# Kernel tuning notes

Hardware: AMD Instinct MI355X
Metric: run time of the kernel (lower is better)

## Reference

```python
import jax, jax.numpy as jnp
import numpy as np

N = 16777216  # length of the returns series


def setup_inputs() -> dict:
    key = jax.random.key(0)
    returns = 0.01 * jax.random.normal(key, (N,), dtype=jnp.float32)
    return {
        "returns": returns,
        "omega": jnp.float32(0.01),
        "alpha": jnp.float32(0.1),
        "beta": jnp.float32(0.85),
    }


def reference(returns, omega, alpha, beta):
    # GARCH(1,1): h[0] = var(returns) (unbiased, matching torch.var default);
    # h[t] = omega + alpha * r[t-1]^2 + beta * h[t-1]
    h0 = jnp.var(returns, ddof=1)
    # drivers b_t = omega + alpha * r_{t-1}^2 for t = 1..n-1
    b = omega + alpha * jnp.square(returns[:-1])

    def step(h_prev, b_t):
        h_t = b_t + beta * h_prev
        return h_t, h_t

    _, h_rest = jax.lax.scan(step, h0, b)
    h = jnp.concatenate([h0[None], h_rest])  # [n]
    return jnp.sqrt(h), h
```

## Files before the change

kernel.cpp:

```cpp
#include <hip/hip_runtime.h>
#include <math.h>


#define VAR_BLOCKS 1024
#define KPW 4096
#define MAIN_BLOCK 256

__global__ void var_partial(const float* __restrict__ r, int n,
                            double* __restrict__ partial) {
    int tid = blockIdx.x * blockDim.x + threadIdx.x;
    int stride = gridDim.x * blockDim.x;
    double s = 0.0, q = 0.0;
    int n4 = n >> 2;
    const float4* r4 = (const float4*)r;
    for (int i = tid; i < n4; i += stride) {
        float4 v = r4[i];
        s += (double)v.x + (double)v.y + (double)v.z + (double)v.w;
        q += (double)v.x * v.x + (double)v.y * v.y
           + (double)v.z * v.z + (double)v.w * v.w;
    }
    for (int i = (n4 << 2) + tid; i < n; i += stride) {
        double v = r[i];
        s += v; q += v * v;
    }
    for (int d = 1; d < 64; d <<= 1) {
        s += __shfl_xor(s, d, 64);
        q += __shfl_xor(q, d, 64);
    }
    __shared__ double ls[4], lq[4];
    int wid = threadIdx.x >> 6, lane = threadIdx.x & 63;
    if (lane == 0) { ls[wid] = s; lq[wid] = q; }
    __syncthreads();
    if (threadIdx.x == 0) {
        double S = 0.0, Q = 0.0;
        for (int w = 0; w < (int)(blockDim.x >> 6); ++w) { S += ls[w]; Q += lq[w]; }
        partial[2 * blockIdx.x]     = S;
        partial[2 * blockIdx.x + 1] = Q;
    }
}

__global__ void var_final(const double* __restrict__ partial, int nblocks, int n,
                          float* __restrict__ h0_out) {
    double s = 0.0, q = 0.0;
    for (int i = threadIdx.x; i < nblocks; i += blockDim.x) {
        s += partial[2 * i];
        q += partial[2 * i + 1];
    }
    for (int d = 1; d < 64; d <<= 1) {
        s += __shfl_xor(s, d, 64);
        q += __shfl_xor(q, d, 64);
    }
    __shared__ double ls[4], lq[4];
    int wid = threadIdx.x >> 6, lane = threadIdx.x & 63;
    if (lane == 0) { ls[wid] = s; lq[wid] = q; }
    __syncthreads();
    if (threadIdx.x == 0) {
        double S = 0.0, Q = 0.0;
        for (int w = 0; w < (int)(blockDim.x >> 6); ++w) { S += ls[w]; Q += lq[w]; }
        double mean = S / (double)n;
        double var = (Q - (double)n * mean * mean) / (double)(n - 1);
        *h0_out = (float)var;
    }
}

__global__ __launch_bounds__(MAIN_BLOCK)
void garch_main(const float* __restrict__ r, int n,
                const float* __restrict__ pOmega, const float* __restrict__ pAlpha,
                const float* __restrict__ pBeta, const float* __restrict__ pH0,
                float* __restrict__ out_sqrt, float* __restrict__ out_h) {
    const int lane = threadIdx.x & 63;
    const int gwave = (blockIdx.x * blockDim.x + threadIdx.x) >> 6;
    const int start = gwave * KPW;
    if (start >= n) return;

    const float omega = *pOmega;
    const float alpha = *pAlpha;
    const float beta  = *pBeta;
    const float h0    = *pH0;

    const float c1 = beta;
    const float c2 = c1 * c1;
    const float c3 = c2 * c1;
    const float c4 = c2 * c2;
    const float c8 = c4 * c4;
    const float c16 = c8 * c8;
    const float c32 = c16 * c16;
    const float c64 = c32 * c32;
    const float c128 = c64 * c64;

    float pw1 = 1.0f;
    {
        float p = beta; int e = lane;
        if (e & 1)  pw1 *= p; p *= p;
        if (e & 2)  pw1 *= p; p *= p;
        if (e & 4)  pw1 *= p; p *= p;
        if (e & 8)  pw1 *= p; p *= p;
        if (e & 16) pw1 *= p; p *= p;
        if (e & 32) pw1 *= p;
    }
    float pw4 = 1.0f;
    {
        float p = c4; int e = lane;
        if (e & 1)  pw4 *= p; p *= p;
        if (e & 2)  pw4 *= p; p *= p;
        if (e & 4)  pw4 *= p; p *= p;
        if (e & 8)  pw4 *= p; p *= p;
        if (e & 16) pw4 *= p; p *= p;
        if (e & 32) pw4 *= p;
    }

    float h_prev, r_carry;
    if (start == 0) {
        h_prev = 0.0f;
        r_carry = 0.0f;
    } else {
        float ra = r[start - 2 - lane];
        float rb = r[start - 66 - lane];
        float ba = fmaf(alpha * ra, ra, omega);
        float bb = fmaf(alpha * rb, rb, omega);
        float part = pw1 * fmaf(c64, bb, ba);
        for (int d = 1; d < 64; d <<= 1) part += __shfl_xor(part, d, 64);
        h_prev = part;
        r_carry = r[start - 1];
    }

    int end = start + KPW; if (end > n) end = n;
    const float4* r4p = (const float4*)r;

    int s = start;
    for (; s + 256 <= end; s += 256) {
        float4 rv = r4p[(s >> 2) + lane];
        float prev = __shfl_up(rv.w, 1, 64);
        if (lane == 0) prev = r_carry;

        float b0 = fmaf(alpha * prev, prev, omega);
        float b1 = fmaf(alpha * rv.x, rv.x, omega);
        float b2 = fmaf(alpha * rv.y, rv.y, omega);
        float b3 = fmaf(alpha * rv.z, rv.z, omega);
        if (s == 0 && lane == 0) b0 = h0;

        float B = fmaf(c1, b2, b3);
        B = fmaf(c2, b1, B);
        B = fmaf(c3, b0, B);

        float t;
        t = __shfl_up(B, 1, 64);  if (lane >= 1)  B = fmaf(c4,  t, B);
        t = __shfl_up(B, 2, 64);  if (lane >= 2)  B = fmaf(c8,  t, B);
        t = __shfl_up(B, 4, 64);  if (lane >= 4)  B = fmaf(c16, t, B);
        t = __shfl_up(B, 8, 64);  if (lane >= 8)  B = fmaf(c32, t, B);
        t = __shfl_up(B, 16, 64); if (lane >= 16) B = fmaf(c64, t, B);
        t = __shfl_up(B, 32, 64); if (lane >= 32) B = fmaf(c128, t, B);

        float Bex = __shfl_up(B, 1, 64);
        if (lane == 0) Bex = 0.0f;
        float h_base = fmaf(pw4, h_prev, Bex);

        float h0v = fmaf(c1, h_base, b0);
        float h1v = fmaf(c1, h0v, b1);
        float h2v = fmaf(c1, h1v, b2);
        float h3v = fmaf(c1, h2v, b3);

        int idx4 = (s >> 2) + lane;
        float4 hs = make_float4(h0v, h1v, h2v, h3v);
        float4 sq = make_float4(sqrtf(h0v), sqrtf(h1v), sqrtf(h2v), sqrtf(h3v));
        reinterpret_cast<float4*>(out_sqrt)[idx4] = sq;
        reinterpret_cast<float4*>(out_h)[idx4]    = hs;

        h_prev  = __shfl(h3v, 63, 64);
        r_carry = __shfl(rv.w, 63, 64);
    }

    if (s < end && lane == 0) {
        float h = h_prev;
        for (int tt = s; tt < end; ++tt) {
            float rr = (tt > 0) ? r[tt - 1] : 0.0f;
            float b = fmaf(alpha * rr, rr, omega);
            float hv = (tt == 0) ? h0 : fmaf(beta, h, b);
            out_sqrt[tt] = sqrtf(hv);
            out_h[tt] = hv;
            h = hv;
        }
    }
}

extern "C" void kernel_launch(void* const* d_in, const int* in_sizes, int n_in,
                              void* d_out, int out_size, void* d_ws, size_t ws_size,
                              hipStream_t stream) {
    const float* r      = (const float*)d_in[0];
    const float* pOmega = (const float*)d_in[1];
    const float* pAlpha = (const float*)d_in[2];
    const float* pBeta  = (const float*)d_in[3];
    int n = in_sizes[0];

    float* out_sqrt = (float*)d_out;
    float* out_h    = out_sqrt + n;

    double* partial = (double*)d_ws;
    float* h0p = (float*)((char*)d_ws + 2 * VAR_BLOCKS * sizeof(double));

    var_partial<<<VAR_BLOCKS, 256, 0, stream>>>(r, n, partial);
    var_final<<<1, 256, 0, stream>>>(partial, VAR_BLOCKS, n, h0p);

    int elems_per_block = KPW * (MAIN_BLOCK / 64);
    int nblocks = (n + elems_per_block - 1) / elems_per_block;
    garch_main<<<nblocks, MAIN_BLOCK, 0, stream>>>(
        r, n, pOmega, pAlpha, pBeta, h0p, out_sqrt, out_h);
}
```

Baseline: 196.9 us.

## Fuse variance reduction into scan pass and patch the h0-dependent prefix afterward

Drops the separate variance pre-pass so the input is read once. The scan kernel now also accumulates the sum and sum of squares. It runs with h0 treated as zero, and a single-block finalize kernel computes the variance and serially recomputes the first 256 outputs, where beta^t*h0 still matters in float. Each wave now handles 8 elements per lane with nontemporal stores. The risk is that truncating the h0 correction at 256 steps relies on beta^256 being negligible, which holds for typical beta but is not exact in general.

```diff
diff --git a/kernel.cpp b/kernel.cpp
--- a/kernel.cpp
+++ b/kernel.cpp
@@ -2,34 +2,161 @@
 #include <math.h>
 
 
-#define VAR_BLOCKS 1024
-#define KPW 4096
+#define KPW 2048
 #define MAIN_BLOCK 256
-
-__global__ void var_partial(const float* __restrict__ r, int n,
-                            double* __restrict__ partial) {
-    int tid = blockIdx.x * blockDim.x + threadIdx.x;
-    int stride = gridDim.x * blockDim.x;
-    double s = 0.0, q = 0.0;
-    int n4 = n >> 2;
-    const float4* r4 = (const float4*)r;
-    for (int i = tid; i < n4; i += stride) {
-        float4 v = r4[i];
-        s += (double)v.x + (double)v.y + (double)v.z + (double)v.w;
-        q += (double)v.x * v.x + (double)v.y * v.y
-           + (double)v.z * v.z + (double)v.w * v.w;
-    }
-    for (int i = (n4 << 2) + tid; i < n; i += stride) {
-        double v = r[i];
-        s += v; q += v * v;
-    }
+#define FIX 256
+
+typedef float v4f __attribute__((ext_vector_type(4)));
+
+__global__ __launch_bounds__(MAIN_BLOCK, 6)
+void garch_fused(const float* __restrict__ r, int n,
+                 const float* __restrict__ pOmega, const float* __restrict__ pAlpha,
+                 const float* __restrict__ pBeta,
+                 float* __restrict__ out_sqrt, float* __restrict__ out_h,
+                 double* __restrict__ partial) {
+    const int lane = threadIdx.x & 63;
+    const int wid  = threadIdx.x >> 6;
+    const int gwave = (blockIdx.x * blockDim.x + threadIdx.x) >> 6;
+    const int start = gwave * KPW;
+
+    const float omega = *pOmega;
+    const float alpha = *pAlpha;
+    const float beta  = *pBeta;
+
+    const float c1 = beta;
+    const float c2 = c1 * c1;
+    const float c3 = c2 * c1;
+    const float c4 = c2 * c2;
+    const float c8 = c4 * c4;
+    const float c16 = c8 * c8;
+    const float c32 = c16 * c16;
+    const float c64 = c32 * c32;
+    const float c128 = c64 * c64;
+    const float c256 = c128 * c128;
+
+    double acc_s = 0.0, acc_q = 0.0;
+
+    if (start < n) {
+        float pw1 = 1.0f;
+        { float p = c1; int e = lane;
+          if (e & 1)  pw1 *= p; p *= p;
+          if (e & 2)  pw1 *= p; p *= p;
+          if (e & 4)  pw1 *= p; p *= p;
+          if (e & 8)  pw1 *= p; p *= p;
+          if (e & 16) pw1 *= p; p *= p;
+          if (e & 32) pw1 *= p; }
+        float pw8 = 1.0f;
+        { float p = c8; int e = lane;
+          if (e & 1)  pw8 *= p; p *= p;
+          if (e & 2)  pw8 *= p; p *= p;
+          if (e & 4)  pw8 *= p; p *= p;
+          if (e & 8)  pw8 *= p; p *= p;
+          if (e & 16) pw8 *= p; p *= p;
+          if (e & 32) pw8 *= p; }
+
+        float h_prev, r_carry;
+        if (start == 0) {
+            h_prev = 0.0f;
+            r_carry = 0.0f;
+        } else {
+            float ra = r[start - 2 - lane];
+            float rb = r[start - 66 - lane];
+            float ba = fmaf(alpha * ra, ra, omega);
+            float bb = fmaf(alpha * rb, rb, omega);
+            float part = pw1 * fmaf(c64, bb, ba);
+            for (int d = 1; d < 64; d <<= 1) part += __shfl_xor(part, d, 64);
+            h_prev = part;
+            r_carry = r[start - 1];
+        }
+
+        int end = start + KPW; if (end > n) end = n;
+        const float4* r4p = (const float4*)r;
+
+        int s = start;
+        for (; s + 512 <= end; s += 512) {
+            int idx4 = (s >> 2) + 2 * lane;
+            float4 ra = r4p[idx4];
+            float4 rb = r4p[idx4 + 1];
+
+            float sf = ((ra.x + ra.y) + (ra.z + ra.w)) + ((rb.x + rb.y) + (rb.z + rb.w));
+            float qf = fmaf(ra.x, ra.x, fmaf(ra.y, ra.y, fmaf(ra.z, ra.z, ra.w * ra.w)));
+            qf = fmaf(rb.x, rb.x, fmaf(rb.y, rb.y, fmaf(rb.z, rb.z, fmaf(rb.w, rb.w, qf))));
+            acc_s += (double)sf;
+            acc_q += (double)qf;
+
+            float prev = __shfl_up(rb.w, 1, 64);
+            if (lane == 0) prev = r_carry;
+
+            float b0 = fmaf(alpha * prev, prev, omega);
+            float b1 = fmaf(alpha * ra.x, ra.x, omega);
+            float b2 = fmaf(alpha * ra.y, ra.y, omega);
+            float b3 = fmaf(alpha * ra.z, ra.z, omega);
+            float b4 = fmaf(alpha * ra.w, ra.w, omega);
+            float b5 = fmaf(alpha * rb.x, rb.x, omega);
+            float b6 = fmaf(alpha * rb.y, rb.y, omega);
+            float b7 = fmaf(alpha * rb.z, rb.z, omega);
+            if (s == 0 && lane == 0) b0 = 0.0f;
+
+            float lo = fmaf(c1, b2, b3); lo = fmaf(c2, b1, lo); lo = fmaf(c3, b0, lo);
+            float B  = fmaf(c1, b6, b7); B  = fmaf(c2, b5, B);  B  = fmaf(c3, b4, B);
+            B = fmaf(c4, lo, B);
+
+            float t;
+            t = __shfl_up(B, 1, 64);  if (lane >= 1)  B = fmaf(c8,   t, B);
+            t = __shfl_up(B, 2, 64);  if (lane >= 2)  B = fmaf(c16,  t, B);
+            t = __shfl_up(B, 4, 64);  if (lane >= 4)  B = fmaf(c32,  t, B);
+            t = __shfl_up(B, 8, 64);  if (lane >= 8)  B = fmaf(c64,  t, B);
+            t = __shfl_up(B, 16, 64); if (lane >= 16) B = fmaf(c128, t, B);
+            t = __shfl_up(B, 32, 64); if (lane >= 32) B = fmaf(c256, t, B);
+
+            float Bex = __shfl_up(B, 1, 64);
+            if (lane == 0) Bex = 0.0f;
+            float h_base = fmaf(pw8, h_prev, Bex);
+
+            float h0v = fmaf(c1, h_base, b0);
+            float h1v = fmaf(c1, h0v, b1);
+            float h2v = fmaf(c1, h1v, b2);
+            float h3v = fmaf(c1, h2v, b3);
+            float h4v = fmaf(c1, h3v, b4);
+            float h5v = fmaf(c1, h4v, b5);
+            float h6v = fmaf(c1, h5v, b6);
+            float h7v = fmaf(c1, h6v, b7);
+
+            v4f hA = {h0v, h1v, h2v, h3v};
+            v4f hB = {h4v, h5v, h6v, h7v};
+            v4f sA = {sqrtf(h0v), sqrtf(h1v), sqrtf(h2v), sqrtf(h3v)};
+            v4f sB = {sqrtf(h4v), sqrtf(h5v), sqrtf(h6v), sqrtf(h7v)};
+            __builtin_nontemporal_store(hA, (v4f*)out_h + idx4);
+            __builtin_nontemporal_store(hB, (v4f*)out_h + idx4 + 1);
+            __builtin_nontemporal_store(sA, (v4f*)out_sqrt + idx4);
+            __builtin_nontemporal_store(sB, (v4f*)out_sqrt + idx4 + 1);
+
+            h_prev  = __shfl(h7v, 63, 64);
+            r_carry = __shfl(rb.w, 63, 64);
+        }
+
+        if (s < end && lane == 0) {
+            float h = h_prev;
+            for (int tt = s; tt < end; ++tt) {
+                float rr = (tt > 0) ? r[tt - 1] : 0.0f;
+                float b = fmaf(alpha * rr, rr, omega);
+                float hv = (tt == 0) ? 0.0f : fmaf(beta, h, b);
+                out_sqrt[tt] = sqrtf(hv);
+                out_h[tt] = hv;
+                h = hv;
+                float rv = r[tt];
+                acc_s += (double)rv;
+                acc_q += (double)rv * rv;
+            }
+        }
+    }
+
     for (int d = 1; d < 64; d <<= 1) {
-        s += __shfl_xor(s, d, 64);
-        q += __shfl_xor(q, d, 64);
-    }
-    __shared__ double ls[4], lq[4];
-    int wid = threadIdx.x >> 6, lane = threadIdx.x & 63;
-    if (lane == 0) { ls[wid] = s; lq[wid] = q; }
+        acc_s += __shfl_xor(acc_s, d, 64);
+        acc_q += __shfl_xor(acc_q, d, 64);
+    }
+    __shared__ double ls[MAIN_BLOCK / 64], lq[MAIN_BLOCK / 64];
+    if (lane == 0) { ls[wid] = acc_s; lq[wid] = acc_q; }
     __syncthreads();
     if (threadIdx.x == 0) {
         double S = 0.0, Q = 0.0;
@@ -39,8 +166,16 @@
     }
 }
 
-__global__ void var_final(const double* __restrict__ partial, int nblocks, int n,
-                          float* __restrict__ h0_out) {
+__global__ void garch_finalize(const double* __restrict__ partial, int nblocks, int n,
+                               const float* __restrict__ r,
+                               const float* __restrict__ pOmega,
+                               const float* __restrict__ pAlpha,
+                               const float* __restrict__ pBeta,
+                               float* __restrict__ out_sqrt, float* __restrict__ out_h) {
+    __shared__ float rbuf[FIX];
+    int fix = (n < FIX) ? n : FIX;
+    for (int i = threadIdx.x; i < fix - 1; i += blockDim.x) rbuf[i] = r[i];
+
     double s = 0.0, q = 0.0;
     for (int i = threadIdx.x; i < nblocks; i += blockDim.x) {
         s += partial[2 * i];
@@ -59,126 +194,17 @@
         for (int w = 0; w < (int)(blockDim.x >> 6); ++w) { S += ls[w]; Q += lq[w]; }
         double mean = S / (double)n;
         double var = (Q - (double)n * mean * mean) / (double)(n - 1);
-        *h0_out = (float)var;
-    }
-}
-
-__global__ __launch_bounds__(MAIN_BLOCK)
-void garch_main(const float* __restrict__ r, int n,
-                const float* __restrict__ pOmega, const float* __restrict__ pAlpha,
-                const float* __restrict__ pBeta, const float* __restrict__ pH0,
-                float* __restrict__ out_sqrt, float* __restrict__ out_h) {
-    const int lane = threadIdx.x & 63;
-    const int gwave = (blockIdx.x * blockDim.x + threadIdx.x) >> 6;
-    const int start = gwave * KPW;
-    if (start >= n) return;
-
-    const float omega = *pOmega;
-    const float alpha = *pAlpha;
-    const float beta  = *pBeta;
-    const float h0    = *pH0;
-
-    const float c1 = beta;
-    const float c2 = c1 * c1;
-    const float c3 = c2 * c1;
-    const float c4 = c2 * c2;
-    const float c8 = c4 * c4;
-    const float c16 = c8 * c8;
-    const float c32 = c16 * c16;
-    const float c64 = c32 * c32;
-    const float c128 = c64 * c64;
-
-    float pw1 = 1.0f;
-    {
-        float p = beta; int e = lane;
-        if (e & 1)  pw1 *= p; p *= p;
-        if (e & 2)  pw1 *= p; p *= p;
-        if (e & 4)  pw1 *= p; p *= p;
-        if (e & 8)  pw1 *= p; p *= p;
-        if (e & 16) pw1 *= p; p *= p;
-        if (e & 32) pw1 *= p;
-    }
-    float pw4 = 1.0f;
-    {
-        float p = c4; int e = lane;
-        if (e & 1)  pw4 *= p; p *= p;
-        if (e & 2)  pw4 *= p; p *= p;
-        if (e & 4)  pw4 *= p; p *= p;
-        if (e & 8)  pw4 *= p; p *= p;
-        if (e & 16) pw4 *= p; p *= p;
-        if (e & 32) pw4 *= p;
-    }
-
-    float h_prev, r_carry;
-    if (start == 0) {
-        h_prev = 0.0f;
-        r_carry = 0.0f;
-    } else {
-        float ra = r[start - 2 - lane];
-        float rb = r[start - 66 - lane];
-        float ba = fmaf(alpha * ra, ra, omega);
-        float bb = fmaf(alpha * rb, rb, omega);
-        float part = pw1 * fmaf(c64, bb, ba);
-        for (int d = 1; d < 64; d <<= 1) part += __shfl_xor(part, d, 64);
-        h_prev = part;
-        r_carry = r[start - 1];
-    }
-
-    int end = start + KPW; if (end > n) end = n;
-    const float4* r4p = (const float4*)r;
-
-    int s = start;
-    for (; s + 256 <= end; s += 256) {
-        float4 rv = r4p[(s >> 2) + lane];
-        float prev = __shfl_up(rv.w, 1, 64);
-        if (lane == 0) prev = r_carry;
-
-        float b0 = fmaf(alpha * prev, prev, omega);
-        float b1 = fmaf(alpha * rv.x, rv.x, omega);
-        float b2 = fmaf(alpha * rv.y, rv.y, omega);
-        float b3 = fmaf(alpha * rv.z, rv.z, omega);
-        if (s == 0 && lane == 0) b0 = h0;
-
-        float B = fmaf(c1, b2, b3);
-        B = fmaf(c2, b1, B);
-        B = fmaf(c3, b0, B);
-
-        float t;
-        t = __shfl_up(B, 1, 64);  if (lane >= 1)  B = fmaf(c4,  t, B);
-        t = __shfl_up(B, 2, 64);  if (lane >= 2)  B = fmaf(c8,  t, B);
-        t = __shfl_up(B, 4, 64);  if (lane >= 4)  B = fmaf(c16, t, B);
-        t = __shfl_up(B, 8, 64);  if (lane >= 8)  B = fmaf(c32, t, B);
-        t = __shfl_up(B, 16, 64); if (lane >= 16) B = fmaf(c64, t, B);
-        t = __shfl_up(B, 32, 64); if (lane >= 32) B = fmaf(c128, t, B);
-
-        float Bex = __shfl_up(B, 1, 64);
-        if (lane == 0) Bex = 0.0f;
-        float h_base = fmaf(pw4, h_prev, Bex);
-
-        float h0v = fmaf(c1, h_base, b0);
-        float h1v = fmaf(c1, h0v, b1);
-        float h2v = fmaf(c1, h1v, b2);
-        float h3v = fmaf(c1, h2v, b3);
-
-        int idx4 = (s >> 2) + lane;
-        float4 hs = make_float4(h0v, h1v, h2v, h3v);
-        float4 sq = make_float4(sqrtf(h0v), sqrtf(h1v), sqrtf(h2v), sqrtf(h3v));
-        reinterpret_cast<float4*>(out_sqrt)[idx4] = sq;
-        reinterpret_cast<float4*>(out_h)[idx4]    = hs;
-
-        h_prev  = __shfl(h3v, 63, 64);
-        r_carry = __shfl(rv.w, 63, 64);
-    }
-
-    if (s < end && lane == 0) {
-        float h = h_prev;
-        for (int tt = s; tt < end; ++tt) {
-            float rr = (tt > 0) ? r[tt - 1] : 0.0f;
+        float h0 = (float)var;
+        float omega = *pOmega, alpha = *pAlpha, beta = *pBeta;
+
+        float h = h0;
+        if (n > 0) { out_h[0] = h; out_sqrt[0] = sqrtf(h); }
+        for (int t = 1; t < fix; ++t) {
+            float rr = rbuf[t - 1];
             float b = fmaf(alpha * rr, rr, omega);
-            float hv = (tt == 0) ? h0 : fmaf(beta, h, b);
-            out_sqrt[tt] = sqrtf(hv);
-            out_h[tt] = hv;
-            h = hv;
+            h = fmaf(beta, h, b);
+            out_h[t] = h;
+            out_sqrt[t] = sqrtf(h);
         }
     }
 }
@@ -196,13 +222,12 @@
     float* out_h    = out_sqrt + n;
 
     double* partial = (double*)d_ws;
-    float* h0p = (float*)((char*)d_ws + 2 * VAR_BLOCKS * sizeof(double));
-
-    var_partial<<<VAR_BLOCKS, 256, 0, stream>>>(r, n, partial);
-    var_final<<<1, 256, 0, stream>>>(partial, VAR_BLOCKS, n, h0p);
 
     int elems_per_block = KPW * (MAIN_BLOCK / 64);
     int nblocks = (n + elems_per_block - 1) / elems_per_block;
-    garch_main<<<nblocks, MAIN_BLOCK, 0, stream>>>(
-        r, n, pOmega, pAlpha, pBeta, h0p, out_sqrt, out_h);
+
+    garch_fused<<<nblocks, MAIN_BLOCK, 0, stream>>>(
+        r, n, pOmega, pAlpha, pBeta, out_sqrt, out_h, partial);
+    garch_finalize<<<1, 256, 0, stream>>>(
+        partial, nblocks, n, r, pOmega, pAlpha, pBeta, out_sqrt, out_h);
 }
```

Result: slower. 253.2 us (+28.6%).
